# Kernel optimization log

Hardware: AMD Instinct MI355X
Metric: run time of the kernel (lower is better)

The kernel has to match this reference:

```python
import jax, jax.numpy as jnp
import numpy as np

NEG_SLOPE = 0.02

def setup_inputs() -> dict:
    key = jax.random.key(0)
    ks = jax.random.split(key, 6)
    B, C, H, W = 32, 64, 128, 128
    K, L, OUT = 1000, 12, 24
    x = jax.random.normal(ks[0], (B, C, H, W), dtype=jnp.float32)
    pos = jax.random.randint(ks[1], (K, B, L, 2), 0, 128, dtype=jnp.int32)
    # middle: Conv2d(C, C, 3, stride=1, padding=1)
    conv_w = jax.random.normal(ks[2], (C, C, 3, 3), dtype=jnp.float32) * (1.0 / np.sqrt(C * 9))
    conv_b = jax.random.normal(ks[3], (C,), dtype=jnp.float32) * 0.01
    # predictor: Linear(C*L, OUT), kaiming init, zero bias
    pred_w = jax.random.normal(ks[4], (OUT, C * L), dtype=jnp.float32) * np.sqrt(2.0 / (C * L))
    pred_b = jnp.zeros((OUT,), dtype=jnp.float32)
    return {"x": x, "pos": pos, "conv_w": conv_w, "conv_b": conv_b, "pred_w": pred_w, "pred_b": pred_b}

def reference(x, pos, conv_w, conv_b, pred_w, pred_b):
    # middle conv (3x3, same padding) + LeakyReLU(0.02)
    h = jax.lax.conv_general_dilated(
        x, conv_w, window_strides=(1, 1), padding=((1, 1), (1, 1)),
        dimension_numbers=("NCHW", "OIHW", "NCHW")) + conv_b[None, :, None, None]
    h = jnp.where(h > 0, h, NEG_SLOPE * h)  # [B,C,H,W]
    B, C, H, W = h.shape
    K, _, L, _ = pos.shape
    # clamp coords and build flattened spatial indices
    px = jnp.clip(pos[..., 0], 0, W - 1)
    py = jnp.clip(pos[..., 1], 0, H - 1)
    idx = (py * W + px).transpose(1, 0, 2)           # [B,K,L]
    hf = h.reshape(B, C, H * W).transpose(0, 2, 1)   # [B,HW,C]
    # irregular gather: per-batch pick L spatial locations for K candidates
    kernel_seq = hf[jnp.arange(B)[:, None, None], idx]  # [B,K,L,C]
    kernel_seq = kernel_seq.reshape(B, K, L * C)
    out = kernel_seq @ pred_w.T + pred_b             # [B,K,OUT]
    return out.transpose(1, 0, 2)                    # [K,B,OUT]
```

## Files before the change

### kernel.cpp

```cpp
#include <hip/hip_runtime.h>
#include <hip/hip_bf16.h>

typedef __attribute__((ext_vector_type(8))) short short8;
typedef __attribute__((ext_vector_type(4))) float f32x4;

#define NEG_SLOPE 0.02f

static __device__ __forceinline__ unsigned short f2bf(float f) {
    unsigned int u = __float_as_uint(f);
    u += 0x7fffu + ((u >> 16) & 1u);
    return (unsigned short)(u >> 16);
}

static __device__ __forceinline__ unsigned int pk2bf(float lo, float hi) {
    __hip_bfloat162 t = __float22bfloat162_rn(float2{lo, hi});
    unsigned int u;
    __builtin_memcpy(&u, &t, 4);
    return u;
}

static __device__ __forceinline__ void gld_lds16(const unsigned short* g, unsigned short* l) {
    __builtin_amdgcn_global_load_lds(
        (const __attribute__((address_space(1))) unsigned int*)g,
        (__attribute__((address_space(3))) unsigned int*)(void*)l,
        16, 0, 0);
}

#define WROW 304
#define ROW_BYTES 8320

__global__ __launch_bounds__(256) void prep_kernel(const float* __restrict__ conv_w,
                                                   const float* __restrict__ pred_w,
                                                   unsigned short* __restrict__ wb,
                                                   unsigned short* __restrict__ pwb) {
    int i = blockIdx.x * 256 + threadIdx.x;
    if (i < 2 * 64 * WROW) {
        int cc = i / (64 * WROW);
        int rem = i - cc * (64 * WROW);
        int co = rem / WROW, e = rem - co * WROW;
        float v = 0.0f;
        if (e < 288) {
            int tap = e >> 5, ci5 = e & 31;
            v = conv_w[(co * 64 + cc * 32 + ci5) * 9 + tap];
        }
        wb[i] = f2bf(v);
    }
    if (i < 24576) {
        int o = i / 768, k = i - o * 768;
        pwb[i] = f2bf(o < 24 ? pred_w[o * 768 + k] : 0.0f);
    }
}

__global__ __launch_bounds__(512, 4) void conv_mfma(const float* __restrict__ x,
                                                    const unsigned short* __restrict__ wb,
                                                    const float* __restrict__ cb,
                                                    unsigned short* __restrict__ h) {
    __shared__ unsigned short w_sm[64 * WROW];
    __shared__ unsigned char in_sm[4 * ROW_BYTES];

    const int id = blockIdx.x;
    const int xcd = id & 7, local = id >> 3;
    const int b = local & 31;
    const int y0 = ((xcd << 3) + (local >> 5)) * 2;

    const int tid = threadIdx.x;
    const int wave = tid >> 6, lane = tid & 63;
    const int lr = lane & 15, kg = lane >> 4;
    const int ro = wave >> 2;
    const int px0 = (wave & 3) * 32;
    const int y = y0 + ro;

    f32x4 acc[2][4];
#pragma unroll
    for (int m = 0; m < 2; ++m)
#pragma unroll
        for (int n = 0; n < 4; ++n) acc[m][n] = (f32x4){0.f, 0.f, 0.f, 0.f};

    const unsigned char* ab[2][3];
#pragma unroll
    for (int m = 0; m < 2; ++m)
#pragma unroll
        for (int dx = 0; dx < 3; ++dx) {
            int xx = px0 + m * 16 + lr + dx;
            int pair = xx >> 1, odd = xx & 1;
            int slot = ((odd << 2) | kg) ^ (pair & 7);
            ab[m][dx] = in_sm + pair * 128 + slot * 16;
        }
    const unsigned short* bbp[4];
#pragma unroll
    for (int n = 0; n < 4; ++n) bbp[n] = w_sm + (n * 16 + lr) * WROW + kg * 8;

    const int p_ = tid & 63, q_ = (tid >> 6) & 3, rr_ = tid >> 8;
    const int slotA = (4 | q_) ^ (p_ & 7);
    const int dstA = p_ * 128 + slotA * 16;
    const int slotB = q_ ^ ((p_ + 1) & 7);
    const int dstB = (p_ + 1) * 128 + slotB * 16;

    float2 F[2][8];

#define LOADX(CCI)                                                                 \
    {                                                                              \
        const float* xq_ = x + ((size_t)b * 64 + (CCI) * 32 + q_ * 8) * 16384;     \
        _Pragma("unroll")                                                          \
        for (int pass = 0; pass < 2; ++pass) {                                     \
            const int r_ = pass * 2 + rr_;                                         \
            const int gy_ = y0 + r_ - 1;                                           \
            if ((unsigned)gy_ < 128u) {                                            \
                const float* s_ = xq_ + gy_ * 128 + 2 * p_;                        \
                _Pragma("unroll")                                                  \
                for (int c = 0; c < 8; ++c)                                        \
                    F[pass][c] = *(const float2*)(s_ + (size_t)c * 16384);         \
            } else {                                                               \
                _Pragma("unroll")                                                  \
                for (int c = 0; c < 8; ++c) F[pass][c] = (float2){0.f, 0.f};       \
            }                                                                      \
        }                                                                          \
    }

#define STOREX()                                                                   \
    {                                                                              \
        _Pragma("unroll")                                                          \
        for (int pass = 0; pass < 2; ++pass) {                                     \
            const int r_ = pass * 2 + rr_;                                         \
            uint4 Av, Bv;                                                          \
            Av.x = pk2bf(F[pass][0].x, F[pass][1].x);                              \
            Av.y = pk2bf(F[pass][2].x, F[pass][3].x);                              \
            Av.z = pk2bf(F[pass][4].x, F[pass][5].x);                              \
            Av.w = pk2bf(F[pass][6].x, F[pass][7].x);                              \
            Bv.x = pk2bf(F[pass][0].y, F[pass][1].y);                              \
            Bv.y = pk2bf(F[pass][2].y, F[pass][3].y);                              \
            Bv.z = pk2bf(F[pass][4].y, F[pass][5].y);                              \
            Bv.w = pk2bf(F[pass][6].y, F[pass][7].y);                              \
            *(uint4*)(in_sm + r_ * ROW_BYTES + dstA) = Av;                         \
            *(uint4*)(in_sm + r_ * ROW_BYTES + dstB) = Bv;                         \
        }                                                                          \
    }

#define STAGEW(CCI)                                                                \
    {                                                                              \
        const unsigned short* wsrc_ = wb + (CCI) * (64 * WROW);                    \
        _Pragma("unroll")                                                          \
        for (int j0 = 0; j0 < 2560; j0 += 512) {                                   \
            int j_ = j0 + tid;                                                     \
            if (j_ < 2432) gld_lds16(wsrc_ + j_ * 8, w_sm + j_ * 8);               \
        }                                                                          \
    }

#define TAILZ()                                                                    \
    if (tid < 32) {                                                                \
        int q = tid & 3, r = (tid >> 2) & 3, which = tid >> 4;                     \
        int dst = which == 0 ? (q * 16) : (64 * 128 + (4 | q) * 16);               \
        *(uint4*)(in_sm + r * ROW_BYTES + dst) = (uint4){0u, 0u, 0u, 0u};          \
    }

#define COMPUTE()                                                                  \
    _Pragma("unroll")                                                              \
    for (int t = 0; t < 9; ++t) {                                                  \
        const int dy = t / 3, dx = t % 3;                                          \
        const int aoff = (ro + dy) * ROW_BYTES;                                    \
        short8 A0 = *(const short8*)(ab[0][dx] + aoff);                            \
        short8 A1 = *(const short8*)(ab[1][dx] + aoff);                            \
        _Pragma("unroll")                                                          \
        for (int n = 0; n < 4; ++n) {                                              \
            short8 B = *(const short8*)(bbp[n] + t * 32);                          \
            acc[0][n] = __builtin_amdgcn_mfma_f32_16x16x32_bf16(A0, B, acc[0][n], 0, 0, 0); \
            acc[1][n] = __builtin_amdgcn_mfma_f32_16x16x32_bf16(A1, B, acc[1][n], 0, 0, 0); \
        }                                                                          \
    }

    LOADX(0)
    STAGEW(0)
    STOREX()
    TAILZ()
    LOADX(1)
    __syncthreads();
    COMPUTE()
    __syncthreads();
    STAGEW(1)
    STOREX()
    TAILZ()
    __syncthreads();
    COMPUTE()

#undef LOADX
#undef STOREX
#undef STAGEW
#undef TAILZ
#undef COMPUTE

    float bias[4];
#pragma unroll
    for (int n = 0; n < 4; ++n) bias[n] = cb[n * 16 + lr];
    const size_t hrow = (size_t)(b * 128 + y) * 128;
#pragma unroll
    for (int m = 0; m < 2; ++m)
#pragma unroll
        for (int rr = 0; rr < 4; ++rr) {
            const int p = px0 + m * 16 + kg * 4 + rr;
            unsigned short* hp = h + (hrow + p) * 64 + lr;
#pragma unroll
            for (int n = 0; n < 4; ++n) {
                float v = acc[m][n][rr] + bias[n];
                v = v > 0.0f ? v : NEG_SLOPE * v;
                hp[n * 16] = f2bf(v);
            }
        }
}

__global__ __launch_bounds__(256, 2) void gather_gemm(const unsigned short* __restrict__ h,
                                                      const int* __restrict__ pos,
                                                      const unsigned short* __restrict__ pw,
                                                      const float* __restrict__ pred_b,
                                                      float* __restrict__ out) {
    __shared__ unsigned char pw_lds[32 * 1536];
    const int tid = threadIdx.x;

    for (int i = tid; i < 3072; i += 256) {
        int row = i / 96, c = i - row * 96;
        int dst = row * 1536 + ((c * 16) ^ ((row & 7) << 4));
        *(uint4*)(pw_lds + dst) = ((const uint4*)pw)[i];
    }
    __syncthreads();

    const int wave = tid >> 6, lane = tid & 63;
    const int pair_base = blockIdx.x * 64 + wave * 16;
    const int prow = lane & 15;
    const int kgrp = lane >> 4;
    const int pair = pair_base + prow;
    const int b = pair & 31;
    const unsigned short* hb = h + (size_t)b * 16384 * 64;

    const int swz0 = (prow & 7) << 4;
    const unsigned char* bro0 = pw_lds + prow * 1536;
    const unsigned char* bro1 = pw_lds + (prow + 16) * 1536;

    f32x4 acc0a = {0.f, 0.f, 0.f, 0.f};
    f32x4 acc1a = {0.f, 0.f, 0.f, 0.f};
    f32x4 acc0b = {0.f, 0.f, 0.f, 0.f};
    f32x4 acc1b = {0.f, 0.f, 0.f, 0.f};

#pragma unroll
    for (int l = 0; l < 12; ++l) {
        int2 pq = ((const int2*)pos)[pair * 12 + l];
        int px = pq.x < 0 ? 0 : (pq.x > 127 ? 127 : pq.x);
        int py = pq.y < 0 ? 0 : (pq.y > 127 ? 127 : pq.y);
        const unsigned short* pix = hb + (((size_t)py << 7) + px) * 64;
#pragma unroll
        for (int half = 0; half < 2; ++half) {
            const int c0 = half * 32 + kgrp * 8;
            short8 a = *(const short8*)(pix + c0);
            const int kb = (l * 64 + half * 32 + kgrp * 8) * 2;
            short8 b0 = *(const short8*)(bro0 + (kb ^ swz0));
            short8 b1 = *(const short8*)(bro1 + (kb ^ swz0));
            if (l < 6) {
                acc0a = __builtin_amdgcn_mfma_f32_16x16x32_bf16(a, b0, acc0a, 0, 0, 0);
                acc1a = __builtin_amdgcn_mfma_f32_16x16x32_bf16(a, b1, acc1a, 0, 0, 0);
            } else {
                acc0b = __builtin_amdgcn_mfma_f32_16x16x32_bf16(a, b0, acc0b, 0, 0, 0);
                acc1b = __builtin_amdgcn_mfma_f32_16x16x32_bf16(a, b1, acc1b, 0, 0, 0);
            }
        }
    }

    const int o0 = lane & 15;
    const float bias0 = pred_b[o0];
    const float bias1 = (o0 + 16 < 24) ? pred_b[o0 + 16] : 0.0f;
#pragma unroll
    for (int r = 0; r < 4; ++r) {
        const int pout = pair_base + (lane >> 4) * 4 + r;
        out[(size_t)pout * 24 + o0] = acc0a[r] + acc0b[r] + bias0;
        if (o0 + 16 < 24)
            out[(size_t)pout * 24 + o0 + 16] = acc1a[r] + acc1b[r] + bias1;
    }
}

extern "C" void kernel_launch(void* const* d_in, const int* in_sizes, int n_in,
                              void* d_out, int out_size, void* d_ws, size_t ws_size,
                              hipStream_t stream) {
    const float* x      = (const float*)d_in[0];
    const int*   pos    = (const int*)d_in[1];
    const float* conv_w = (const float*)d_in[2];
    const float* conv_b = (const float*)d_in[3];
    const float* pred_w = (const float*)d_in[4];
    const float* pred_b = (const float*)d_in[5];
    float* out = (float*)d_out;

    char* ws = (char*)d_ws;
    unsigned short* h   = (unsigned short*)ws;
    unsigned short* wb  = (unsigned short*)(ws + 67108864);
    unsigned short* pwb = (unsigned short*)(ws + 67108864 + 77824);

    prep_kernel<<<152, 256, 0, stream>>>(conv_w, pred_w, wb, pwb);
    conv_mfma<<<2048, 512, 0, stream>>>(x, wb, conv_b, h);
    gather_gemm<<<500, 256, 0, stream>>>(h, pos, pwb, pred_b, out);
}
```

Measured before the change: 84.67 us.

## Split gather-GEMM reduction over L into two halves with a combine kernel

The gather GEMM is split along the L (reduction) dimension into two halves. The grid doubles to 1000 blocks, each holding half of the predictor weights in LDS, and each half writes partial sums to a workspace buffer. A new combine kernel adds the two partials and the bias. The aim is more parallelism and occupancy in the latency-bound gather, at the cost of an extra kernel launch and the write and re-read of about 6 MB of partials.

```diff
diff --git a/kernel.cpp b/kernel.cpp
--- a/kernel.cpp
+++ b/kernel.cpp
@@ -207,23 +207,24 @@
         }
 }
 
-__global__ __launch_bounds__(256, 2) void gather_gemm(const unsigned short* __restrict__ h,
+__global__ __launch_bounds__(256, 2) void gather_half(const unsigned short* __restrict__ h,
                                                       const int* __restrict__ pos,
                                                       const unsigned short* __restrict__ pw,
-                                                      const float* __restrict__ pred_b,
-                                                      float* __restrict__ out) {
-    __shared__ unsigned char pw_lds[32 * 1536];
+                                                      float* __restrict__ P) {
+    __shared__ unsigned char pw_lds[32 * 768];
+    const int bid = blockIdx.x;
+    const int kh = bid & 1, grp = bid >> 1;
     const int tid = threadIdx.x;
 
-    for (int i = tid; i < 3072; i += 256) {
-        int row = i / 96, c = i - row * 96;
-        int dst = row * 1536 + ((c * 16) ^ ((row & 7) << 4));
-        *(uint4*)(pw_lds + dst) = ((const uint4*)pw)[i];
+    for (int i = tid; i < 1536; i += 256) {
+        int row = i / 48, c = i - row * 48;
+        int dst = row * 768 + ((c * 16) ^ ((row & 7) << 4));
+        *(uint4*)(pw_lds + dst) = *(const uint4*)(pw + row * 768 + kh * 384 + c * 8);
     }
     __syncthreads();
 
     const int wave = tid >> 6, lane = tid & 63;
-    const int pair_base = blockIdx.x * 64 + wave * 16;
+    const int pair_base = grp * 64 + wave * 16;
     const int prow = lane & 15;
     const int kgrp = lane >> 4;
     const int pair = pair_base + prow;
@@ -231,8 +232,8 @@
     const unsigned short* hb = h + (size_t)b * 16384 * 64;
 
     const int swz0 = (prow & 7) << 4;
-    const unsigned char* bro0 = pw_lds + prow * 1536;
-    const unsigned char* bro1 = pw_lds + (prow + 16) * 1536;
+    const unsigned char* bro0 = pw_lds + prow * 768;
+    const unsigned char* bro1 = pw_lds + (prow + 16) * 768;
 
     f32x4 acc0a = {0.f, 0.f, 0.f, 0.f};
     f32x4 acc1a = {0.f, 0.f, 0.f, 0.f};
@@ -240,7 +241,8 @@
     f32x4 acc1b = {0.f, 0.f, 0.f, 0.f};
 
 #pragma unroll
-    for (int l = 0; l < 12; ++l) {
+    for (int l6 = 0; l6 < 6; ++l6) {
+        const int l = kh * 6 + l6;
         int2 pq = ((const int2*)pos)[pair * 12 + l];
         int px = pq.x < 0 ? 0 : (pq.x > 127 ? 127 : pq.x);
         int py = pq.y < 0 ? 0 : (pq.y > 127 ? 127 : pq.y);
@@ -249,10 +251,10 @@
         for (int half = 0; half < 2; ++half) {
             const int c0 = half * 32 + kgrp * 8;
             short8 a = *(const short8*)(pix + c0);
-            const int kb = (l * 64 + half * 32 + kgrp * 8) * 2;
+            const int kb = (l6 * 64 + half * 32 + kgrp * 8) * 2;
             short8 b0 = *(const short8*)(bro0 + (kb ^ swz0));
             short8 b1 = *(const short8*)(bro1 + (kb ^ swz0));
-            if (l < 6) {
+            if (l6 < 3) {
                 acc0a = __builtin_amdgcn_mfma_f32_16x16x32_bf16(a, b0, acc0a, 0, 0, 0);
                 acc1a = __builtin_amdgcn_mfma_f32_16x16x32_bf16(a, b1, acc1a, 0, 0, 0);
             } else {
@@ -263,14 +265,23 @@
     }
 
     const int o0 = lane & 15;
-    const float bias0 = pred_b[o0];
-    const float bias1 = (o0 + 16 < 24) ? pred_b[o0 + 16] : 0.0f;
+    float* Pp = P + (size_t)kh * 768000;
 #pragma unroll
     for (int r = 0; r < 4; ++r) {
         const int pout = pair_base + (lane >> 4) * 4 + r;
-        out[(size_t)pout * 24 + o0] = acc0a[r] + acc0b[r] + bias0;
+        Pp[(size_t)pout * 24 + o0] = acc0a[r] + acc0b[r];
         if (o0 + 16 < 24)
-            out[(size_t)pout * 24 + o0 + 16] = acc1a[r] + acc1b[r] + bias1;
+            Pp[(size_t)pout * 24 + o0 + 16] = acc1a[r] + acc1b[r];
+    }
+}
+
+__global__ __launch_bounds__(256) void combine_kernel(const float* __restrict__ P,
+                                                      const float* __restrict__ pred_b,
+                                                      float* __restrict__ out) {
+    int i = blockIdx.x * 256 + threadIdx.x;
+    if (i < 768000) {
+        int o = i % 24;
+        out[i] = P[i] + P[i + 768000] + pred_b[o];
     }
 }
 
@@ -289,8 +300,10 @@
     unsigned short* h   = (unsigned short*)ws;
     unsigned short* wb  = (unsigned short*)(ws + 67108864);
     unsigned short* pwb = (unsigned short*)(ws + 67108864 + 77824);
+    float*          P   = (float*)(ws + 67108864 + 77824 + 49152);
 
     prep_kernel<<<152, 256, 0, stream>>>(conv_w, pred_w, wb, pwb);
     conv_mfma<<<2048, 512, 0, stream>>>(x, wb, conv_b, h);
-    gather_gemm<<<500, 256, 0, stream>>>(h, pos, pwb, pred_b, out);
-}
+    gather_half<<<1000, 256, 0, stream>>>(h, pos, pwb, P);
+    combine_kernel<<<3000, 256, 0, stream>>>(P, pred_b, out);
+}
```

Result: slower. 87.13 us (+2.9%).
